# Performance work log

Hardware: AMD Instinct MI355X
Metric: run time of the kernel (lower is better)

Reference implementation:

```python
import jax, jax.numpy as jnp
import numpy as np
from math import ceil

N, C_IN, HV, WV = 4, 3, 256, 256
C, K, NUM_LAYERS = 16, 3, 10
HK, WK = 45, 45
PROX_SCALE, KSCALE, KBSCALE, EPS = 10.0, 100.0, 0.01, 1e-8


def conv2_same(x, w):
    # torch F.conv2d (cross-correlation) with 'same' padding
    return jax.lax.conv_general_dilated(x, w, (1, 1), 'SAME',
                                        dimension_numbers=('NCHW', 'OIHW', 'NCHW'))


def pad_to(x, size):
    h, w = x.shape[-2], x.shape[-1]
    pads = [(0, 0)] * (x.ndim - 2) + [(0, size[0] - h), (0, size[1] - w)]
    return jnp.pad(x, pads)


def soft_threshold(x, b):
    return jnp.sign(x) * jax.nn.relu(jnp.abs(x) - b)


def circ_shift(x, s):
    return jnp.roll(x, (-s[0], -s[1]), axis=(-2, -1))


def csq(c):
    return (c * jnp.conj(c)).real


def forward(blurred_image, w0, ws, biases, kernel_biases, kernel_proxes, zetas, eta):
    Nb, C_in, Hv, Wv = blurred_image.shape
    Hs, Ws = Hv + HK - 1, Wv + WK - 1
    Hb, Wb = Hs + HK - 1, Ws + WK - 1
    fft_size = (int(ceil(Hb / 64.0) * 64), int(ceil(Wb / 64.0) * 64))
    rfft = lambda x: jnp.fft.rfft2(x, s=fft_size, axes=(-2, -1))
    irfft = lambda X: jnp.fft.irfft2(X, s=fft_size, axes=(-2, -1))

    # first-layer filter: zero-mean per (out,in) filter, then spatial reflect
    w_mean = w0.reshape(C, C_in, -1).mean(axis=-1)
    w0c = w0 - w_mean[:, :, None, None]
    w0_unreflected = jnp.transpose(w0c, (1, 0, 2, 3))   # (C_in, C, K, K)
    w0r = w0c[:, :, ::-1, ::-1]

    # analysis: cascade of convs, each feature stack padded to fft_size
    wy_list = []
    fy = blurred_image
    for layer in range(NUM_LAYERS):
        w = w0r if layer == 0 else ws[layer - 1]
        fy = conv2_same(fy, w)
        fy_p = pad_to(jnp.pad(fy, ((0, 0), (0, 0), (HK - 1, HK - 1), (WK - 1, WK - 1))), fft_size)
        wy_list.append(fy_p)

    delta = jnp.zeros((Nb, HK, WK), dtype=blurred_image.dtype).at[:, HK // 2, WK // 2].set(1.0)
    b0 = biases[0][None, :, None, None]
    z = soft_threshold(circ_shift(wy_list[-1], (HK // 2, WK // 2)), b0)
    Fz = rfft(z)
    k = delta
    Fg = None
    for layer in range(NUM_LAYERS):
        fy_p = wy_list.pop()
        Ffy = rfft(fy_p)                       # (N, C, H, Wf) complex
        Fk = rfft(k)[:, None]                  # (N, 1, H, Wf)
        zeta = PROX_SCALE * zetas[layer][None, :, None, None]
        num = zeta * (jnp.conj(Fk) * Ffy) + Fz
        den = zeta * csq(Fk) + 1.0
        Fg = num / (den + EPS)
        b = biases[layer + 1][None, :, None, None]
        z = soft_threshold(irfft(Fg), b)
        Fz = rfft(z)
        zk = kernel_proxes[layer]
        num_k = zk * jnp.sum(jnp.conj(Fz) * Ffy, axis=1) + Fk[:, 0]
        den_k = zk * jnp.sum(csq(Fz), axis=1) + 1.0
        k = irfft(num_k / (den_k + EPS))
        k_flat = k.reshape(Nb, -1)
        k_max = jax.scipy.special.logsumexp(k_flat * KSCALE, axis=-1) / KSCALE
        bk = KBSCALE * kernel_biases[layer]
        k = jax.nn.relu(k[:, :HK, :WK] - bk * k_max[:, None, None])
        k_sum = jnp.sum(k, axis=(1, 2), keepdims=True)
        k = (k + EPS * delta) / (k_sum + EPS)

    # final closed-form image solve in frequency domain (3-channel Cramer's rule)
    Fy = rfft(jnp.pad(blurred_image, ((0, 0), (0, 0), (HK - 1, HK - 1), (WK - 1, WK - 1))))
    Fk = rfft(k)                                # (N, H, Wf)
    Fw0 = rfft(circ_shift(pad_to(w0_unreflected, fft_size), (K // 2, K // 2)))  # (C_in, C, H, Wf)
    b_final = biases[NUM_LAYERS + 1][None, :, None, None]
    Fg = rfft(soft_threshold(irfft(Fg), b_final))

    eta_s = PROX_SCALE * eta[None, :, None, None]      # (1, C, 1, 1)
    Fwr, Fwg, Fwb = Fw0[0:1], Fw0[1:2], Fw0[2:3]       # (1, C, H, Wf)
    Fyr, Fyg, Fyb = Fy[:, 0], Fy[:, 1], Fy[:, 2]
    Fk_sq = csq(Fk)
    Crr = Fk_sq + jnp.sum(eta_s * csq(Fwr), axis=1)
    Cgg = Fk_sq + jnp.sum(eta_s * csq(Fwg), axis=1)
    Cbb = Fk_sq + jnp.sum(eta_s * csq(Fwb), axis=1)
    Crg = jnp.sum(eta_s * jnp.conj(Fwr) * Fwg, axis=1)
    Crb = jnp.sum(eta_s * jnp.conj(Fwr) * Fwb, axis=1)
    Cgb = jnp.sum(eta_s * jnp.conj(Fwg) * Fwb, axis=1)
    Fk_conj = jnp.conj(Fk)
    Br = Fk_conj * Fyr + jnp.sum(eta_s * jnp.conj(Fwr) * Fg, axis=1)
    Bg = Fk_conj * Fyg + jnp.sum(eta_s * jnp.conj(Fwg) * Fg, axis=1)
    Bb = Fk_conj * Fyb + jnp.sum(eta_s * jnp.conj(Fwb) * Fg, axis=1)
    Crg_sq, Crb_sq, Cgb_sq = csq(Crg), csq(Crb), csq(Cgb)
    Irr = Cgg * Cbb - Cgb_sq
    Igg = Crr * Cbb - Crb_sq
    Ibb = Crr * Cgg - Crg_sq
    Irg = jnp.conj(Cgb) * Crb - Cbb * Crg
    Irb = Crg * Cgb - Cgg * Crb
    Igb = jnp.conj(Crg) * Crb - Crr * Cgb
    den = (Crr * (Cgg * Cbb - Cgb_sq) - Cgg * Crb_sq - Cbb * Crg_sq
           + 2 * (Crg * Cgb * jnp.conj(Crb)).real) + EPS
    Fxr = Irr * Br + Irg * Bg + Irb * Bb
    Fxg = jnp.conj(Irg) * Br + Igg * Bg + Igb * Bb
    Fxb = jnp.conj(Irb) * Br + jnp.conj(Igb) * Bg + Ibb * Bb
    Fx = jnp.stack([Fxr, Fxg, Fxb], axis=1) / den[:, None]

    image = irfft(Fx)[:, :, HK // 2:HK // 2 + Hv, WK // 2:WK // 2 + Wv]
    return image, k


def setup_inputs() -> dict:
    key = jax.random.key(0)
    ks = jax.random.split(key, 4)

    def xavier(k, shape, fan_in, fan_out):
        std = (2.0 / (fan_in + fan_out)) ** 0.5
        return std * jax.random.normal(k, shape, dtype=jnp.float32)

    return {
        'blurred_image': jax.random.normal(ks[0], (N, C_IN, HV, WV), dtype=jnp.float32),
        'w0': xavier(ks[1], (C, C_IN, K, K), C_IN * K * K, C * K * K),
        'ws': xavier(ks[2], (NUM_LAYERS - 1, C, C, 3, 3), C * 9, C * 9),
        'biases': jnp.full((NUM_LAYERS + 2, C), 0.02, dtype=jnp.float32),
        'kernel_biases': jnp.zeros((NUM_LAYERS,), dtype=jnp.float32),
        'kernel_proxes': jnp.ones((NUM_LAYERS,), dtype=jnp.float32),
        'zetas': jnp.ones((NUM_LAYERS, C), dtype=jnp.float32),
        'eta': jnp.ones((C,), dtype=jnp.float32),
    }


def reference(blurred_image, w0, ws, biases, kernel_biases, kernel_proxes, zetas, eta):
    return forward(blurred_image, w0, ws, biases, kernel_biases, kernel_proxes, zetas, eta)
```

## Files before the change

kernel.cpp:

```cpp
#include <hip/hip_runtime.h>
#include <math.h>

#define FH 384
#define KF 193
#define SPW 147456

typedef __attribute__((ext_vector_type(8))) short short8;
typedef __attribute__((ext_vector_type(4))) float f32x4;
typedef unsigned int u32;
typedef unsigned short u16;

static __device__ __forceinline__ float softt(float v, float b) {
    return copysignf(fmaxf(fabsf(v) - b, 0.f), v);
}
static __device__ __forceinline__ u16 bf16_rn(float v) {
    u32 u = __float_as_uint(v);
    u32 r = (u + 0x7FFFu + ((u >> 16) & 1u)) >> 16;
    return (u16)r;
}
static __device__ __forceinline__ float bf16_to_f(u16 h) {
    return __uint_as_float(((u32)h) << 16);
}
static __device__ __forceinline__ float2 ldc(const uint2* __restrict__ S, size_t i) {
    uint2 u = S[i];
    float2 r;
    r.x = __uint_as_float((u.x & 0xffffu) << 16) + __uint_as_float((u.y & 0xffffu) << 16);
    r.y = __uint_as_float(u.x & 0xffff0000u) + __uint_as_float(u.y & 0xffff0000u);
    return r;
}
static __device__ __forceinline__ float2 ldcu(uint2 u) {
    float2 r;
    r.x = __uint_as_float((u.x & 0xffffu) << 16) + __uint_as_float((u.y & 0xffffu) << 16);
    r.y = __uint_as_float(u.x & 0xffff0000u) + __uint_as_float(u.y & 0xffff0000u);
    return r;
}
static __device__ __forceinline__ uint2 packc(float re, float im) {
    u16 hr = bf16_rn(re), hi = bf16_rn(im);
    u16 lr = bf16_rn(re - bf16_to_f(hr)), li = bf16_rn(im - bf16_to_f(hi));
    uint2 o; o.x = (u32)hr | ((u32)hi << 16); o.y = (u32)lr | ((u32)li << 16);
    return o;
}
static __device__ __forceinline__ float2 cmul(float2 a, float2 b) {
    float2 r; r.x = a.x*b.x - a.y*b.y; r.y = a.x*b.y + a.y*b.x; return r;
}

__global__ void init_ef_k(float2* Ef) {
    int idx = blockIdx.x * 256 + threadIdx.x;
    if (idx >= FH * FH) return;
    int h = idx / FH, j = idx % FH;
    int m = (h * j) % FH;
    float th = (float)(6.283185307179586 / FH) * (float)m;
    float2 v; v.x = cosf(th); v.y = -sinf(th);
    Ef[idx] = v;
}

__global__ void init_tw(float2* twT) {
    int i = blockIdx.x * 256 + threadIdx.x;
    if (i < 193) {
        float th = (float)(6.283185307179586 / 384.0) * (float)i;
        float2 v; v.x = cosf(th); v.y = sinf(th);
        twT[i] = v;
    }
}

__global__ void init_e96(u16* __restrict__ H, u16* __restrict__ L, int inv)
{
    int idx = blockIdx.x * 256 + threadIdx.x;
    if (idx >= 192 * 192) return;
    int gm = idx / 192, kp = idx % 192;
    int m = gm >> 1, comp = gm & 1;
    int t = kp >> 1, ri = kp & 1;
    int mm = (m * t) % 96;
    float th = (float)(6.283185307179586 / 96.0) * (float)mm;
    float c = cosf(th), s = sinf(th);
    float er, ei;
    if (inv) { er = c * (1.f/384.f); ei = s * (1.f/384.f); }
    else     { er = c;               ei = -s; }
    float v;
    if (comp == 0) v = (ri == 0) ? er : -ei;
    else           v = (ri == 0) ? ei :  er;
    u16 h = bf16_rn(v);
    H[idx] = h;
    L[idx] = bf16_rn(v - bf16_to_f(h));
}

__global__ void init_t192(u16* __restrict__ H, u16* __restrict__ L)
{
    int idx = blockIdx.x * 256 + threadIdx.x;
    if (idx >= 208 * 192) return;
    int n = idx / 192, m = idx % 192;
    float v = 0.f;
    if (n < 194) {
        int j = n >> 1, ri = n & 1;
        int mm = (j * m) % 192;
        float th = (float)(6.283185307179586 / 192.0) * (float)mm;
        v = ri ? -sinf(th) : cosf(th);
    }
    u16 h = bf16_rn(v);
    H[idx] = h;
    L[idx] = bf16_rn(v - bf16_to_f(h));
}

__global__ void init_u192(u16* __restrict__ H, u16* __restrict__ L)
{
    int idx = blockIdx.x * 256 + threadIdx.x;
    if (idx >= 192 * 224) return;
    int m = idx / 224, kk = idx % 224;
    float v = 0.f;
    if (kk < 194) {
        int j = kk >> 1, ri = kk & 1;
        float cj = (j == 0 || j == 96) ? (1.f/384.f) : (2.f/384.f);
        int mm = (j * m) % 192;
        float th = (float)(6.283185307179586 / 192.0) * (float)mm;
        v = ri ? -cj*sinf(th) : cj*cosf(th);
    }
    u16 h = bf16_rn(v);
    H[idx] = h;
    L[idx] = bf16_rn(v - bf16_to_f(h));
}

__global__ void w0c_kernel(const float* __restrict__ w0, float* __restrict__ w0c) {
    int t = threadIdx.x;
    if (t < 48) {
        float m = 0.f;
        for (int d = 0; d < 9; ++d) m += w0[t*9+d];
        m *= (1.f/9.f);
        for (int d = 0; d < 9; ++d) w0c[t*9+d] = w0[t*9+d] - m;
    }
}

__global__ __launch_bounds__(256) void conv3x3_kernel(
    const float* __restrict__ inpF0, const u16* __restrict__ inH0, const u16* __restrict__ inL0,
    const float* __restrict__ w,
    u16* __restrict__ outH0, u16* __restrict__ outL0, int Cin, int flip,
    size_t inImgStride)
{
    size_t iofs = (size_t)blockIdx.z * inImgStride;
    const float* inF = inpF0 ? inpF0 + iofs : nullptr;
    const u16*   iH  = inH0 ? inH0 + iofs : nullptr;
    const u16*   iL  = inL0 ? inL0 + iofs : nullptr;
    u16* oH = outH0 + (size_t)blockIdx.z * 16*65536;
    u16* oL = outL0 + (size_t)blockIdx.z * 16*65536;
    __shared__ float tile[18][19];
    __shared__ float wl[16*16*9];
    int x0 = blockIdx.x * 16, y0 = blockIdx.y * 16;
    int t = threadIdx.x;
    int tx = t & 15, ty = t >> 4;
    int nw = 16 * Cin * 9;
    for (int i = t; i < nw; i += 256) {
        int d = i % 9;
        wl[i] = flip ? w[i + 8 - 2*d] : w[i];
    }
    float acc[16];
#pragma unroll
    for (int co = 0; co < 16; ++co) acc[co] = 0.f;
    for (int ci = 0; ci < Cin; ++ci) {
        __syncthreads();
        for (int i = t; i < 18*18; i += 256) {
            int yy = i / 18, xx = i % 18;
            int gy = y0 - 1 + yy, gx = x0 - 1 + xx;
            float v = 0.f;
            if (gy >= 0 && gy < 256 && gx >= 0 && gx < 256) {
                size_t ii;
                if (inF) ii = ((size_t)ci*256 + gy)*256 + gx;
                else     ii = ((size_t)ci*256 + gy)*256 + ((gx>>1) + (gx&1)*128);
                v = inF ? inF[ii] : (bf16_to_f(iH[ii]) + bf16_to_f(iL[ii]));
            }
            tile[yy][xx] = v;
        }
        __syncthreads();
        float v[9];
#pragma unroll
        for (int dy = 0; dy < 3; dy++)
#pragma unroll
            for (int dx = 0; dx < 3; dx++) v[dy*3+dx] = tile[ty+dy][tx+dx];
#pragma unroll
        for (int co = 0; co < 16; co++) {
            const float* wp = &wl[(co*Cin+ci)*9];
            acc[co] += v[0]*wp[0]+v[1]*wp[1]+v[2]*wp[2]
                     + v[3]*wp[3]+v[4]*wp[4]+v[5]*wp[5]
                     + v[6]*wp[6]+v[7]*wp[7]+v[8]*wp[8];
        }
    }
    int xo = x0 + tx;
    int xd = (xo >> 1) + (xo & 1)*128;
#pragma unroll
    for (int co = 0; co < 16; co++) {
        size_t o = ((size_t)co*256 + (y0+ty))*256 + xd;
        u16 h = bf16_rn(acc[co]);
        oH[o] = h;
        oL[o] = bf16_rn(acc[co] - bf16_to_f(h));
    }
}

__global__ void zinit_kernel(const u16* __restrict__ fy9H, const u16* __restrict__ fy9L,
                             const float* __restrict__ b0,
                             u16* __restrict__ oH, u16* __restrict__ oL, int total)
{
    int idx = blockIdx.x*256 + threadIdx.x;
    if (idx >= total) return;
    int x = idx % FH; int r = idx / FH; int y = r % FH; int plane = r / FH;
    int c = plane & 15;
    int Y = y + 22; if (Y >= FH) Y -= FH;
    int X = x + 22; if (X >= FH) X -= FH;
    int yy = Y - 44, xx = X - 44;
    float v = 0.f;
    if (yy >= 0 && yy < 256 && xx >= 0 && xx < 256) {
        size_t ii = ((size_t)plane*256 + yy)*256 + ((xx>>1) + (xx&1)*128);
        v = bf16_to_f(fy9H[ii]) + bf16_to_f(fy9L[ii]);
    }
    float s = softt(v, b0[c]);
    u16 h = bf16_rn(s);
    size_t d = (size_t)plane*SPW + (size_t)y*FH + ((x>>1) + (x&1)*192);
    oH[d] = h;
    oL[d] = bf16_rn(s - bf16_to_f(h));
}

static __device__ __forceinline__ void r2c192_epilogue(
    f32x4 accA[2][4], f32x4 accB[2][4],
    int col0, int njN, int y0, int wave, int lm, int lq,
    const float2* __restrict__ twT,
    uint2* __restrict__ outp, int B, int plane)
{
#pragma unroll
    for (int mi = 0; mi < 2; ++mi) {
#pragma unroll
// ... 230 lines not shown
    int idx = blockIdx.x*256 + threadIdx.x;
    if (idx >= rows * 97) return;
    int j = idx % 97;
    size_t b = (size_t)(idx / 97) * KF;
    if (j == 96) {
        float2 f = ldc(S, b + 96);
        S[b + 96] = packc(2.f*f.x, -2.f*f.y);
    } else {
        float2 f1 = ldc(S, b + j);
        float2 f2 = ldc(S, b + 192 - j);
        float gpx = f1.x + f2.x, gpy = f1.y - f2.y;
        float hx  = f1.x - f2.x, hy  = f1.y + f2.y;
        float2 tw = twT[j];
        float gmx = tw.x*hx - tw.y*hy;
        float gmy = tw.x*hy + tw.y*hx;
        S[b + j]       = packc(gpx, gpy);
        S[b + 192 - j] = packc(gmx, gmy);
    }
}

template<bool FUSE_LSE>
__global__ __launch_bounds__(256) void c2r192(
    const uint2* __restrict__ Ain,
    const u16* __restrict__ UH, const u16* __restrict__ UL,
    float* __restrict__ outp, const float* __restrict__ thr,
    u16* __restrict__ spH, u16* __restrict__ spL, int B,
    float2* __restrict__ parts)
{
    __shared__ u16 AhS[2][8*64*8];
    __shared__ u16 AlS[2][8*64*8];
    int col0 = blockIdx.x * 64;
    int y0   = blockIdx.y * 128;
    int plane = blockIdx.z;
    int tid = threadIdx.x;
    int wave = tid >> 6, lane = tid & 63;
    int lm = lane & 15, lq = lane >> 4;
    f32x4 accP[2][4], accQ[2][4];
#pragma unroll
    for (int mi = 0; mi < 2; ++mi)
#pragma unroll
        for (int nj = 0; nj < 4; ++nj) {
            accP[mi][nj] = (f32x4){0.f,0.f,0.f,0.f};
            accQ[mi][nj] = (f32x4){0.f,0.f,0.f,0.f};
        }
    for (int kt = 0; kt < 194; kt += 32) {
#pragma unroll
        for (int s = 0; s < 8; ++s) {
            int slot = tid + s*256;
            int p   = slot >> 10;
            int inr = slot & 1023;
            int r = inr >> 3, kq = inr & 7;
            size_t rowb = ((size_t)(y0 + r)*B + plane)*KF;
            int j0 = (kt + kq*4) >> 1;
            uint2 u0, u1;
            u0.x = u0.y = u1.x = u1.y = 0u;
            if (p == 0) {
                if (j0 < 96) u0 = Ain[rowb + j0];
                else if (j0 == 96) {
                    uint2 t = Ain[rowb + 96];
                    u0.x = t.x & 0xffffu; u0.y = t.y & 0xffffu;
                }
                if (j0 + 1 < 96) u1 = Ain[rowb + j0 + 1];
            } else {
                if (j0 < 96) u0 = Ain[rowb + 192 - j0];
                else if (j0 == 96) {
                    uint2 t = Ain[rowb + 96];
                    u0.x = t.x >> 16; u0.y = t.y >> 16;
                }
                if (j0 + 1 < 96) u1 = Ain[rowb + 191 - j0];
            }
            int base = ((r >> 4)*64 + (r & 15) + 16*(kq >> 1))*8 + (kq & 1)*4;
            uint2 hp, lp;
            hp.x = u0.x; hp.y = u1.x;
            lp.x = u0.y; lp.y = u1.y;
            *(uint2*)&AhS[p][base] = hp;
            *(uint2*)&AlS[p][base] = lp;
        }
        __syncthreads();
        short8 A0h[2], A0l[2], A1h[2], A1l[2];
#pragma unroll
        for (int mi = 0; mi < 2; ++mi) {
            int fo = ((wave*2 + mi)*64 + lane)*8;
            A0h[mi] = *(const short8*)&AhS[0][fo];
            A0l[mi] = *(const short8*)&AlS[0][fo];
            A1h[mi] = *(const short8*)&AhS[1][fo];
            A1l[mi] = *(const short8*)&AlS[1][fo];
        }
#pragma unroll
        for (int nj = 0; nj < 4; ++nj) {
            size_t toff = (size_t)(col0 + nj*16 + lm)*224 + kt + lq*8;
            short8 Bh = *(const short8*)(UH + toff);
            short8 Bl = *(const short8*)(UL + toff);
#pragma unroll
            for (int mi = 0; mi < 2; ++mi) {
                accP[mi][nj] = __builtin_amdgcn_mfma_f32_16x16x32_bf16(A0h[mi], Bh, accP[mi][nj], 0, 0, 0);
                accP[mi][nj] = __builtin_amdgcn_mfma_f32_16x16x32_bf16(A0h[mi], Bl, accP[mi][nj], 0, 0, 0);
                accP[mi][nj] = __builtin_amdgcn_mfma_f32_16x16x32_bf16(A0l[mi], Bh, accP[mi][nj], 0, 0, 0);
                accQ[mi][nj] = __builtin_amdgcn_mfma_f32_16x16x32_bf16(A1h[mi], Bh, accQ[mi][nj], 0, 0, 0);
                accQ[mi][nj] = __builtin_amdgcn_mfma_f32_16x16x32_bf16(A1h[mi], Bl, accQ[mi][nj], 0, 0, 0);
                accQ[mi][nj] = __builtin_amdgcn_mfma_f32_16x16x32_bf16(A1l[mi], Bh, accQ[mi][nj], 0, 0, 0);
            }
        }
        __syncthreads();
    }
    float bthr = thr ? thr[plane & 15] : 0.f;
    float lm_ = -1e30f, ls_ = 0.f;
#pragma unroll
    for (int mi = 0; mi < 2; ++mi) {
#pragma unroll
        for (int nj = 0; nj < 4; ++nj) {
            int m = col0 + nj*16 + lm;
#pragma unroll
            for (int rr = 0; rr < 4; ++rr) {
                int y = y0 + wave*32 + mi*16 + lq*4 + rr;
                float xe = accP[mi][nj][rr];
                float xo = accQ[mi][nj][rr];
                float2 o2; o2.x = xe; o2.y = xo;
                *(float2*)&outp[((size_t)plane*FH + y)*FH + 2*m] = o2;
                if (spH) {
                    float s0 = softt(xe, bthr), s1 = softt(xo, bthr);
                    u16 h0 = bf16_rn(s0), h1 = bf16_rn(s1);
                    u16 l0 = bf16_rn(s0 - bf16_to_f(h0)), l1 = bf16_rn(s1 - bf16_to_f(h1));
                    size_t d = (size_t)plane*SPW + (size_t)y*FH + m;
                    spH[d]       = h0; spL[d]       = l0;
                    spH[d + 192] = h1; spL[d + 192] = l1;
                }
                if (FUSE_LSE) {
                    lse_comb(lm_, ls_, 100.f*xe, 1.f);
                    lse_comb(lm_, ls_, 100.f*xo, 1.f);
                }
            }
        }
    }
    if (FUSE_LSE) {
        __shared__ float sm[256], ss[256];
        sm[tid] = lm_; ss[tid] = ls_;
        __syncthreads();
        for (int st = 128; st > 0; st >>= 1) {
            if (tid < st) {
                float mm = sm[tid], sc = ss[tid];
                lse_comb(mm, sc, sm[tid+st], ss[tid+st]);
                sm[tid] = mm; ss[tid] = sc;
            }
            __syncthreads();
        }
        if (tid == 0) {
            float2 o; o.x = sm[0]; o.y = ss[0];
            parts[plane*9 + blockIdx.y*3 + blockIdx.x] = o;
        }
    }
}

template<bool FUSE_FG>
__global__ __launch_bounds__(256) void zgemm_col_mfma4(
    const u16* __restrict__ EH, const u16* __restrict__ EL,
    const uint2* __restrict__ Bm, uint2* __restrict__ Cm, int N, float sgn,
    int ktHi, const float2* __restrict__ twT,
    uint2* __restrict__ FzFg, const uint2* __restrict__ FkB,
    const float* __restrict__ zet16, int GKF)
{
    __shared__ u16 BhS[4][4*64*8];
    __shared__ u16 BlS[4][4*64*8];
    int col0 = blockIdx.x * 64;
    int row0 = blockIdx.y * 64;
    int tid = threadIdx.x;
    int wave = tid >> 6, lane = tid & 63;
    int lm = lane & 15, lq = lane >> 4;
    f32x4 acc[4][4];
#pragma unroll
    for (int p = 0; p < 4; ++p)
#pragma unroll
        for (int nj = 0; nj < 4; ++nj)
            acc[p][nj] = (f32x4){0.f,0.f,0.f,0.f};
    int arow = row0 + wave*16 + lm;
    for (int kt = 0; kt < ktHi; kt += 32) {
        int tbase = kt >> 1;
#pragma unroll
        for (int s = 0; s < 8; ++s) {
            int slot = tid + s*256;
            int p    = slot >> 9;
            int inr  = slot & 511;
            int pair = inr >> 6;
            int n    = inr & 63;
            int gn   = col0 + n;
            int t0   = tbase + pair*2;
            uint2 u0, u1;
            u0.x = u0.y = u1.x = u1.y = 0u;
            if (gn < N) {
                u0 = Bm[(size_t)(4*t0 + p)*N + gn];
                u1 = Bm[(size_t)(4*t0 + 4 + p)*N + gn];
            }
            int ntile = n >> 4, n0 = n & 15;
            int lrow  = (pair >> 1)*16 + n0;
            int base  = (ntile*64 + lrow)*8 + (pair & 1)*4;
            uint2 hp, lp;
            hp.x = u0.x; hp.y = u1.x;
            lp.x = u0.y; lp.y = u1.y;
            *(uint2*)&BhS[p][base] = hp;
            *(uint2*)&BlS[p][base] = lp;
        }
        __syncthreads();
        short8 Ah, Al;
        {
            size_t aoff = (size_t)arow*192 + kt + lq*8;
            Ah = *(const short8*)(EH + aoff);
            Al = *(const short8*)(EL + aoff);
        }
#pragma unroll
        for (int nj = 0; nj < 4; ++nj) {
#pragma unroll
            for (int p = 0; p < 4; ++p) {
                short8 Bh = *(const short8*)&BhS[p][(nj*64 + lane)*8];
                short8 Bl = *(const short8*)&BlS[p][(nj*64 + lane)*8];
                acc[p][nj] = __builtin_amdgcn_mfma_f32_16x16x32_bf16(Ah, Bh, acc[p][nj], 0, 0, 0);
                acc[p][nj] = __builtin_amdgcn_mfma_f32_16x16x32_bf16(Ah, Bl, acc[p][nj], 0, 0, 0);
                acc[p][nj] = __builtin_amdgcn_mfma_f32_16x16x32_bf16(Al, Bh, acc[p][nj], 0, 0, 0);
            }
        }
        __syncthreads();
    }
#pragma unroll
    for (int nj = 0; nj < 4; ++nj) {
        int coln = col0 + nj*16 + lm;
        if (coln < N) {
            int r0 = row0 + wave*16 + lq*4;
            int h0b = r0 >> 1;
            int kk = 0, imgI = 0;
            float zeta = 0.f;
            if (FUSE_FG) {
                int planeI = coln / KF;
                kk = coln - planeI*KF;
                imgI = planeI >> 4;
                zeta = 10.f * zet16[planeI & 15];
            }
#pragma unroll
            for (int pp = 0; pp < 2; ++pp) {
                int h0 = h0b + pp;
                float2 c0, c1, c2, c3;
                c0.x = acc[0][nj][2*pp]; c0.y = acc[0][nj][2*pp+1];
                c1.x = acc[1][nj][2*pp]; c1.y = acc[1][nj][2*pp+1];
                c2.x = acc[2][nj][2*pp]; c2.y = acc[2][nj][2*pp+1];
                c3.x = acc[3][nj][2*pp]; c3.y = acc[3][nj][2*pp+1];
                float2 w1; { float2 t = twT[h0]; w1.x = t.x; w1.y = sgn*t.y; }
                float2 w2 = cmul(w1, w1);
                float2 w3 = cmul(w2, w1);
                float2 d1 = cmul(c1, w1);
                float2 d2 = cmul(c2, w2);
                float2 d3 = cmul(c3, w3);
                float2 s02, m02, s13, m13, i13;
                s02.x = c0.x + d2.x; s02.y = c0.y + d2.y;
                m02.x = c0.x - d2.x; m02.y = c0.y - d2.y;
                s13.x = d1.x + d3.x; s13.y = d1.y + d3.y;
                m13.x = d1.x - d3.x; m13.y = d1.y - d3.y;
                i13.x = -sgn*m13.y;  i13.y = sgn*m13.x;
                float2 X[4];
                X[0].x = s02.x + s13.x; X[0].y = s02.y + s13.y;
                X[2].x = s02.x - s13.x; X[2].y = s02.y - s13.y;
                X[1].x = m02.x + i13.x; X[1].y = m02.y + i13.y;
                X[3].x = m02.x - i13.x; X[3].y = m02.y - i13.y;
#pragma unroll
                for (int q = 0; q < 4; ++q) {
                    int row = h0 + 96*q;
                    uint2 px = packc(X[q].x, X[q].y);
                    Cm[(size_t)row*N + coln] = px;
                    if (FUSE_FG) {
                        float2 fy = ldcu(px);
                        float2 fz = ldc(FzFg, (size_t)row*N + coln);
                        float2 fk = ldc(FkB, (size_t)row*GKF + imgI*KF + kk);
                        float nx = zeta*(fk.x*fy.x + fk.y*fy.y) + fz.x;
                        float ny = zeta*(fk.x*fy.y - fk.y*fy.x) + fz.y;
                        float den = zeta*(fk.x*fk.x + fk.y*fk.y) + 1.f + 1e-8f;
                        float inv = 1.f/den;
                        FzFg[(size_t)row*N + coln] = packc(nx*inv, ny*inv);
                    }
                }
            }
        }
    }
}

__global__ void knum_kernel(const uint2* __restrict__ Fz, const uint2* __restrict__ Ffy,
                            const uint2* __restrict__ Fk, const float* __restrict__ kprox,
                            int L, int total, uint2* __restrict__ outk)
{
    int idx = blockIdx.x*256 + threadIdx.x;
    if (idx >= total) return;
    int k = idx % KF; int r = idx / KF;
    float zk = kprox[L];
    float s1x = 0.f, s1y = 0.f, s2 = 0.f;
    for (int c = 0; c < 16; ++c) {
        size_t bi = ((size_t)r*16 + c)*KF + k;
        float2 fz = ldc(Fz, bi), fy = ldc(Ffy, bi);
        s1x += fz.x*fy.x + fz.y*fy.y;
        s1y += fz.x*fy.y - fz.y*fy.x;
        s2  += fz.x*fz.x + fz.y*fz.y;
    }
    float2 fk = ldc(Fk, idx);
    float nx = zk*s1x + fk.x, ny = zk*s1y + fk.y;
    float den = zk*s2 + 1.f + 1e-8f;
    float inv = 1.f/den;
    outk[idx] = packc(nx*inv, ny*inv);
}

__global__ void zero_kernel(float* __restrict__ p, int n)
{
    int i = blockIdx.x*256 + threadIdx.x;
    if (i < n) p[i] = 0.f;
}

__global__ void kdelta_kernel(float* __restrict__ kful, int G)
{
    int t = threadIdx.x;
    if (t < G) kful[(size_t)t*FH*FH + 22*FH + 22] = 1.f;
}

__global__ __launch_bounds__(256) void knew_kernel(const float2* __restrict__ parts,
    const float* __restrict__ kraw0, const float* __restrict__ kb, int L,
    float* __restrict__ kful0)
{
    int img = blockIdx.x;
    const float* kraw = kraw0 + (size_t)img*FH*FH;
    float*       kful = kful0 + (size_t)img*FH*FH;
    int t = threadIdx.x;
    __shared__ float sm[16], ss[16];
    if (t < 16) {
        if (t < 9) { float2 p = parts[img*9 + t]; sm[t] = p.x; ss[t] = p.y; }
        else       { sm[t] = -1e30f; ss[t] = 0.f; }
    }
    __syncthreads();
    for (int st = 8; st > 0; st >>= 1) {
        if (t < st) {
            float mm = sm[t], sc = ss[t];
            lse_comb(mm, sc, sm[t+st], ss[t+st]);
            sm[t] = mm; ss[t] = sc;
        }
        __syncthreads();
    }
    float kmax = (sm[0] + logf(ss[0])) * 0.01f;
    float thr = 0.01f * kb[L] * kmax;
    float vs[8]; float loc = 0.f;
#pragma unroll
    for (int ii = 0; ii < 8; ++ii) {
        int i = t + ii*256;
        float v = 0.f;
        if (i < 45*45) {
            int y = i/45, x = i - y*45;
            v = fmaxf(kraw[y*FH + x] - thr, 0.f);
        }
        vs[ii] = v; loc += v;
    }
    __shared__ float sr[256];
    sr[t] = loc; __syncthreads();
    for (int st = 128; st > 0; st >>= 1) { if (t < st) sr[t] += sr[t+st]; __syncthreads(); }
    float den = sr[0] + 1e-8f;
#pragma unroll
    for (int ii = 0; ii < 8; ++ii) {
        int i = t + ii*256;
        if (i < 45*45) {
            int y = i/45, x = i - y*45;
            float v = vs[ii] + ((y == 22 && x == 22) ? 1e-8f : 0.f);
            kful[y*FH + x] = v / den;
        }
    }
}

__global__ void fw0_kernel(const float* __restrict__ w0c, const float2* __restrict__ Ef,
                           float2* __restrict__ Fw0)
{
    int idx = blockIdx.x*256 + threadIdx.x;
    if (idx >= 48*FH*KF) return;
    int k = idx % KF; int r = idx / KF;
    int c = r & 15; int r2 = r >> 4;
    int ci = r2 % 3; int h = r2 / 3;
    float accx = 0.f, accy = 0.f;
#pragma unroll
    for (int ky = 0; ky < 3; ++ky) {
        int a1 = ky - 1; if (a1 < 0) a1 += FH;
        float2 e1 = Ef[h*FH + a1];
#pragma unroll
        for (int kx = 0; kx < 3; ++kx) {
            int a2 = kx - 1; if (a2 < 0) a2 += FH;
            float2 e2 = Ef[k*FH + a2];
            float wv = w0c[((c*3 + ci)*3 + ky)*3 + kx];
            float tr = e1.x*e2.x - e1.y*e2.y;
            float ti = e1.x*e2.y + e1.y*e2.x;
            accx += wv*tr; accy += wv*ti;
        }
    }
    float2 o; o.x = accx; o.y = accy;
    Fw0[idx] = o;
}

__global__ void wiener_kernel(const uint2* __restrict__ Fk, const uint2* __restrict__ Fy,
    const float2* __restrict__ Fw0, const uint2* __restrict__ Fg2,
    const float* __restrict__ eta, int G, int total, uint2* __restrict__ Fx)
{
    int idx = blockIdx.x*256 + threadIdx.x;
    if (idx >= total) return;
    int k = idx % KF; int r = idx / KF;
    int h = r / G;
    float2 fk = ldc(Fk, idx);
    float fksq = fk.x*fk.x + fk.y*fk.y;
    float2 fyr = ldc(Fy, ((size_t)3*r + 0)*KF + k);
    float2 fyg = ldc(Fy, ((size_t)3*r + 1)*KF + k);
    float2 fyb = ldc(Fy, ((size_t)3*r + 2)*KF + k);
    float Crr = fksq, Cgg = fksq, Cbb = fksq;
    float2 Crg, Crb, Cgb;
    Crg.x = Crg.y = Crb.x = Crb.y = Cgb.x = Cgb.y = 0.f;
    float2 Br, Bg, Bb;
    Br.x = fk.x*fyr.x + fk.y*fyr.y; Br.y = fk.x*fyr.y - fk.y*fyr.x;
    Bg.x = fk.x*fyg.x + fk.y*fyg.y; Bg.y = fk.x*fyg.y - fk.y*fyg.x;
    Bb.x = fk.x*fyb.x + fk.y*fyb.y; Bb.y = fk.x*fyb.y - fk.y*fyb.x;
    for (int c = 0; c < 16; ++c) {
        float es = 10.f * eta[c];
        float2 wr = Fw0[((size_t)h*48 +  0 + c)*KF + k];
        float2 wg = Fw0[((size_t)h*48 + 16 + c)*KF + k];
        float2 wb = Fw0[((size_t)h*48 + 32 + c)*KF + k];
        float2 g  = ldc(Fg2, ((size_t)r*16 + c)*KF + k);
        Crr += es*(wr.x*wr.x + wr.y*wr.y);
        Cgg += es*(wg.x*wg.x + wg.y*wg.y);
        Cbb += es*(wb.x*wb.x + wb.y*wb.y);
        Crg.x += es*(wr.x*wg.x + wr.y*wg.y); Crg.y += es*(wr.x*wg.y - wr.y*wg.x);
        Crb.x += es*(wr.x*wb.x + wr.y*wb.y); Crb.y += es*(wr.x*wb.y - wr.y*wb.x);
        Cgb.x += es*(wg.x*wb.x + wg.y*wb.y); Cgb.y += es*(wg.x*wb.y - wg.y*wb.x);
        Br.x += es*(wr.x*g.x + wr.y*g.y); Br.y += es*(wr.x*g.y - wr.y*g.x);
        Bg.x += es*(wg.x*g.x + wg.y*g.y); Bg.y += es*(wg.x*g.y - wg.y*g.x);
        Bb.x += es*(wb.x*g.x + wb.y*g.y); Bb.y += es*(wb.x*g.y - wb.y*g.x);
    }
    float Crg_sq = Crg.x*Crg.x + Crg.y*Crg.y;
    float Crb_sq = Crb.x*Crb.x + Crb.y*Crb.y;
    float Cgb_sq = Cgb.x*Cgb.x + Cgb.y*Cgb.y;
    float Irr = Cgg*Cbb - Cgb_sq;
    float Igg = Crr*Cbb - Crb_sq;
    float Ibb = Crr*Cgg - Crg_sq;
    float2 Irg, Irb, Igb;
    Irg.x = (Cgb.x*Crb.x + Cgb.y*Crb.y) - Cbb*Crg.x;
    Irg.y = (Cgb.x*Crb.y - Cgb.y*Crb.x) - Cbb*Crg.y;
    Irb.x = (Crg.x*Cgb.x - Crg.y*Cgb.y) - Cgg*Crb.x;
    Irb.y = (Crg.x*Cgb.y + Crg.y*Cgb.x) - Cgg*Crb.y;
    Igb.x = (Crg.x*Crb.x + Crg.y*Crb.y) - Crr*Cgb.x;
    Igb.y = (Crg.x*Crb.y - Crg.y*Crb.x) - Crr*Cgb.y;
    float tx_ = Crg.x*Cgb.x - Crg.y*Cgb.y;
    float ty_ = Crg.x*Cgb.y + Crg.y*Cgb.x;
    float den = Crr*Irr - Cgg*Crb_sq - Cbb*Crg_sq + 2.f*(tx_*Crb.x + ty_*Crb.y) + 1e-8f;
    float inv = 1.f/den;
    float ox, oy;
    ox = (Irr*Br.x + (Irg.x*Bg.x - Irg.y*Bg.y) + (Irb.x*Bb.x - Irb.y*Bb.y))*inv;
    oy = (Irr*Br.y + (Irg.x*Bg.y + Irg.y*Bg.x) + (Irb.x*Bb.y + Irb.y*Bb.x))*inv;
    Fx[((size_t)3*r + 0)*KF + k] = packc(ox, oy);
    ox = ((Irg.x*Br.x + Irg.y*Br.y) + Igg*Bg.x + (Igb.x*Bb.x - Igb.y*Bb.y))*inv;
    oy = ((Irg.x*Br.y - Irg.y*Br.x) + Igg*Bg.y + (Igb.x*Bb.y + Igb.y*Bb.x))*inv;
    Fx[((size_t)3*r + 1)*KF + k] = packc(ox, oy);
    ox = ((Irb.x*Br.x + Irb.y*Br.y) + (Igb.x*Bg.x + Igb.y*Bg.y) + Ibb*Bb.x)*inv;
    oy = ((Irb.x*Br.y - Irb.y*Br.x) + (Igb.x*Bg.y - Igb.y*Bg.x) + Ibb*Bb.y)*inv;
    Fx[((size_t)3*r + 2)*KF + k] = packc(ox, oy);
}

__global__ void crop_kernel(const float* __restrict__ sp, float* __restrict__ outp, int total)
{
    int idx = blockIdx.x*256 + threadIdx.x;
    if (idx >= total) return;
    int x = idx & 255; int r = idx >> 8; int y = r & 255; int plane = r >> 8;
    outp[idx] = sp[((size_t)plane*FH + (y+22))*FH + (x+22)];
}

__global__ void kcopy_kernel(const float* __restrict__ kful, float* __restrict__ outp, int total)
{
    int idx = blockIdx.x*256 + threadIdx.x;
    if (idx >= total) return;
    int rem = idx % 2025; int img = idx / 2025;
    int x = rem % 45; int y = rem / 45;
    outp[idx] = kful[(size_t)img*FH*FH + y*FH + x];
}

extern "C" void kernel_launch(void* const* d_in, const int* in_sizes, int n_in,
                              void* d_out, int out_size, void* d_ws, size_t ws_size,
                              hipStream_t stream)
{
    (void)in_sizes; (void)n_in; (void)out_size;
    const float* blurred = (const float*)d_in[0];
    const float* w0      = (const float*)d_in[1];
    const float* wsw     = (const float*)d_in[2];
    const float* biases  = (const float*)d_in[3];
    const float* kbias   = (const float*)d_in[4];
    const float* kprox   = (const float*)d_in[5];
    const float* zetas   = (const float*)d_in[6];
    const float* eta     = (const float*)d_in[7];
    float* outp = (float*)d_out;

    auto al = [](size_t b) { return (b + 255) & ~(size_t)255; };
    auto need = [&](int G) -> size_t {
        size_t s = 0;
        s += al((size_t)FH*FH*8);
        s += al(193*8);
        s += 4*al((size_t)192*192*2);
        s += 2*al((size_t)208*192*2);
        s += 2*al((size_t)192*224*2);
        s += al(432*4);
        s += 2*al((size_t)10*G*16*65536*2);
        s += al((size_t)G*16*FH*FH*4);
        s += 2*al((size_t)G*16*SPW*2);
        s += 3*al((size_t)G*16*FH*KF*8);
        s += 4*al((size_t)G*FH*KF*8);
        s += 2*al((size_t)G*FH*FH*4);
        s += 2*al((size_t)G*3*FH*KF*8);
        s += al((size_t)G*64*8);
        return s;
    };
    int G = 4;
    while (G > 1 && need(G) > ws_size) G >>= 1;

    char* base = (char*)d_ws;
    size_t off = 0;
    auto alloc = [&](size_t bytes) -> void* {
        void* p = (void*)(base + off);
        off += (bytes + 255) & ~(size_t)255;
        return p;
    };
    float2* Ef   = (float2*)alloc((size_t)FH*FH*8);
    float2* twT  = (float2*)alloc(193*8);
    u16* EfH = (u16*)alloc((size_t)192*192*2);
    u16* EfL = (u16*)alloc((size_t)192*192*2);
    u16* EiH = (u16*)alloc((size_t)192*192*2);
    u16* EiL = (u16*)alloc((size_t)192*192*2);
    u16* T1H = (u16*)alloc((size_t)208*192*2);
    u16* T1L = (u16*)alloc((size_t)208*192*2);
    u16* U1H = (u16*)alloc((size_t)192*224*2);
    u16* U1L = (u16*)alloc((size_t)192*224*2);
    float*  w0cB = (float*)alloc(432*4);
    u16*    fyH  = (u16*)alloc((size_t)10*G*16*65536*2);
    u16*    fyL  = (u16*)alloc((size_t)10*G*16*65536*2);
    float*  zsp  = (float*)alloc((size_t)G*16*FH*FH*4);
    u16*    zspSH= (u16*)alloc((size_t)G*16*SPW*2);
    u16*    zspSL= (u16*)alloc((size_t)G*16*SPW*2);
    uint2*  mid  = (uint2*)alloc((size_t)G*16*FH*KF*8);
    uint2*  FzFg = (uint2*)alloc((size_t)G*16*FH*KF*8);
    uint2*  Ffy  = (uint2*)alloc((size_t)G*16*FH*KF*8);
    uint2*  Fk   = (uint2*)alloc((size_t)G*FH*KF*8);
    uint2*  kfA  = (uint2*)alloc((size_t)G*FH*KF*8);
    uint2*  kfB  = (uint2*)alloc((size_t)G*FH*KF*8);
    uint2*  kmid = (uint2*)alloc((size_t)G*FH*KF*8);
    float*  kraw = (float*)alloc((size_t)G*FH*FH*4);
    float*  kful = (float*)alloc((size_t)G*FH*FH*4);
    uint2*  FyB  = (uint2*)alloc((size_t)G*3*FH*KF*8);
    uint2*  FxB  = (uint2*)alloc((size_t)G*3*FH*KF*8);
    float2* lseP = (float2*)alloc((size_t)G*64*8);
    float2* Fw0B = (float2*)fyH;

    init_ef_k<<<(FH*FH+255)/256, 256, 0, stream>>>(Ef);
    init_tw<<<1, 256, 0, stream>>>(twT);
    init_e96<<<(192*192+255)/256, 256, 0, stream>>>(EfH, EfL, 0);
    init_e96<<<(192*192+255)/256, 256, 0, stream>>>(EiH, EiL, 1);
    init_t192<<<(208*192+255)/256, 256, 0, stream>>>(T1H, T1L);
    init_u192<<<(192*224+255)/256, 256, 0, stream>>>(U1H, U1L);
    w0c_kernel<<<1, 64, 0, stream>>>(w0, w0cB);

    auto zgf = [&](const uint2* Bm, uint2* Cm, int Ncols) {
        zgemm_col_mfma4<false><<<dim3((Ncols+63)/64, 3), 256, 0, stream>>>(
            EfH, EfL, Bm, Cm, Ncols, -1.f, 192, twT, nullptr, nullptr, nullptr, 0);
    };
    auto zgi = [&](const uint2* Bm, uint2* Cm, int Ncols) {
        zgemm_col_mfma4<false><<<dim3((Ncols+63)/64, 3), 256, 0, stream>>>(
            EiH, EiL, Bm, Cm, Ncols, 1.f, 192, twT, nullptr, nullptr, nullptr, 0);
    };
    auto r2c = [&](const float* inp, int inH, int inW, int oY, int oX,
                   const float* thr, uint2* o, int B) {
        r2c192_f<<<dim3(4, 3, B), 256, 0, stream>>>(
            inp, inH, inW, inW, (size_t)inH*inW, oY, oX, thr, T1H, T1L, twT, o, B);
    };
    auto r2cs = [&](const u16* Hs, const u16* Ls, int inH, int inW, int oY, int oX,
                    uint2* o, int B) {
        r2c192_s<<<dim3(4, 3, B), 256, 0, stream>>>(
            Hs, Ls, inH, inW, oY, oX, T1H, T1L, twT, o, B);
    };
    auto c2r = [&](uint2* Ain, float* o, int B,
                   const float* thr, u16* sH, u16* sL) {
        int rows = FH * B;
        gpm_kernel<<<(rows*97 + 255)/256, 256, 0, stream>>>(Ain, twT, rows);
        c2r192<false><<<dim3(3, 3, B), 256, 0, stream>>>(
            Ain, U1H, U1L, o, thr, sH, sL, B, nullptr);
    };
    auto c2rk = [&](uint2* Ain, float* o, int B, float2* parts) {
        int rows = FH * B;
        gpm_kernel<<<(rows*97 + 255)/256, 256, 0, stream>>>(Ain, twT, rows);
        c2r192<true><<<dim3(3, 3, B), 256, 0, stream>>>(
            Ain, U1H, U1L, o, nullptr, nullptr, nullptr, B, parts);
    };
    auto r2ck = [&]() {
        r2c192_f<<<dim3(4, 1, G), 256, 0, stream>>>(
            kful, 45, 45, FH, (size_t)FH*FH, 0, 0, nullptr, T1H, T1L, twT, kmid, G);
        zgemm_col_mfma4<false><<<dim3((G*KF+63)/64, 3), 256, 0, stream>>>(
            EfH, EfL, kmid, Fk, G*KF, -1.f, 32, twT, nullptr, nullptr, nullptr, 0);
    };

    const size_t CKL = (size_t)G*16*65536;

    for (int g0 = 0; g0 < 4; g0 += G) {
        const float* img = blurred + (size_t)g0*3*65536;

        conv3x3_kernel<<<dim3(16,16,G), 256, 0, stream>>>(
            img, nullptr, nullptr, w0cB, fyH, fyL, 3, 1, (size_t)3*65536);
        for (int l = 1; l < 10; ++l)
            conv3x3_kernel<<<dim3(16,16,G), 256, 0, stream>>>(
                nullptr, fyH + (size_t)(l-1)*CKL, fyL + (size_t)(l-1)*CKL,
                wsw + (size_t)(l-1)*2304,
                fyH + (size_t)l*CKL, fyL + (size_t)l*CKL, 16, 0, (size_t)16*65536);

        int totZ = G*16*FH*FH;
        zinit_kernel<<<(totZ+255)/256, 256, 0, stream>>>(
            fyH + 9*CKL, fyL + 9*CKL, biases, zspSH, zspSL, totZ);
        r2cs(zspSH, zspSL, FH, FH, 0, 0, mid, G*16);
        zgf(mid, FzFg, G*16*KF);

        zero_kernel<<<(G*FH*FH+255)/256, 256, 0, stream>>>(kful, G*FH*FH);
        kdelta_kernel<<<1, 64, 0, stream>>>(kful, G);

        int totK = G*FH*KF;
        int NS = G*16*KF;
        for (int it = 0; it < 10; ++it) {
            int Lfy = 9 - it;
            r2ck();
            r2cs(fyH + (size_t)Lfy*CKL, fyL + (size_t)Lfy*CKL, 256, 256, 44, 44, mid, G*16);
            zgemm_col_mfma4<true><<<dim3((NS+63)/64, 3), 256, 0, stream>>>(
                EfH, EfL, mid, Ffy, NS, -1.f, 192, twT,
                FzFg, Fk, zetas + it*16, G*KF);
            zgi(FzFg, mid, NS);
            c2r(mid, zsp, G*16, biases + (it+1)*16, zspSH, zspSL);
            r2cs(zspSH, zspSL, FH, FH, 0, 0, mid, G*16);
            zgf(mid, FzFg, NS);
            knum_kernel<<<(totK+255)/256, 256, 0, stream>>>(FzFg, Ffy, Fk, kprox, it, totK, kfA);
            zgi(kfA, kfB, G*KF);
            c2rk(kfB, kraw, G, lseP);
            knew_kernel<<<G, 256, 0, stream>>>(lseP, kraw, kbias, it, kful);
        }

        r2c(img, 256, 256, 44, 44, nullptr, mid, 3*G);
        zgf(mid, FyB, 3*G*KF);
        r2ck();
        r2c(zsp, FH, FH, 0, 0, biases + 11*16, mid, G*16);
        zgf(mid, FzFg, G*16*KF);
        fw0_kernel<<<(48*FH*KF+255)/256, 256, 0, stream>>>(w0cB, Ef, Fw0B);
        wiener_kernel<<<(totK+255)/256, 256, 0, stream>>>(Fk, FyB, Fw0B, FzFg, eta, G, totK, FxB);
        zgi(FxB, mid, 3*G*KF);
        c2r(mid, zsp, 3*G, nullptr, nullptr, nullptr);
        int totC = G*3*65536;
        crop_kernel<<<(totC+255)/256, 256, 0, stream>>>(zsp, outp + (size_t)g0*3*65536, totC);
        int totKC = G*2025;
        kcopy_kernel<<<(totKC+255)/256, 256, 0, stream>>>(kful, outp + 786432 + g0*2025, totKC);
    }
}
```

Baseline: 8.136 ms.

## Switch column FFT from 96x4 to 48x8 mixed-radix decomposition

The column-direction 384-point DFT is restructured from a 96-point dense DFT done as an MFMA GEMM plus a radix-4 twiddle stage to a 48-point dense GEMM plus a radix-8 butterfly stage. This halves the K-dimension of the bf16 split-precision GEMM, cutting MFMA work and DFT-matrix traffic, at the cost of a larger butterfly epilogue with more twiddle loads. Tile shapes move to 48x32 blocks with 192 threads, and the twiddle table grows to all 384 entries. The ktHi=32 path for the kernel FFT is kept and still covers the nonzero kernel rows.

```diff
diff --git a/kernel.cpp b/kernel.cpp
--- a/kernel.cpp
+++ b/kernel.cpp
@@ -56,22 +56,22 @@
 
 __global__ void init_tw(float2* twT) {
     int i = blockIdx.x * 256 + threadIdx.x;
-    if (i < 193) {
+    if (i < 384) {
         float th = (float)(6.283185307179586 / 384.0) * (float)i;
         float2 v; v.x = cosf(th); v.y = sinf(th);
         twT[i] = v;
     }
 }
 
-__global__ void init_e96(u16* __restrict__ H, u16* __restrict__ L, int inv)
+__global__ void init_e48(u16* __restrict__ H, u16* __restrict__ L, int inv)
 {
     int idx = blockIdx.x * 256 + threadIdx.x;
-    if (idx >= 192 * 192) return;
-    int gm = idx / 192, kp = idx % 192;
+    if (idx >= 96 * 96) return;
+    int gm = idx / 96, kp = idx % 96;
     int m = gm >> 1, comp = gm & 1;
     int t = kp >> 1, ri = kp & 1;
-    int mm = (m * t) % 96;
-    float th = (float)(6.283185307179586 / 96.0) * (float)mm;
+    int mm = (m * t) % 48;
+    float th = (float)(6.283185307179586 / 48.0) * (float)mm;
     float c = cosf(th), s = sinf(th);
     float er, ei;
     if (inv) { er = c * (1.f/384.f); ei = s * (1.f/384.f); }
@@ -608,43 +608,41 @@
 }
 
 template<bool FUSE_FG>
-__global__ __launch_bounds__(256) void zgemm_col_mfma4(
+__global__ __launch_bounds__(192) void zgemm_col_mfma8(
     const u16* __restrict__ EH, const u16* __restrict__ EL,
     const uint2* __restrict__ Bm, uint2* __restrict__ Cm, int N, float sgn,
     int ktHi, const float2* __restrict__ twT,
     uint2* __restrict__ FzFg, const uint2* __restrict__ FkB,
     const float* __restrict__ zet16, int GKF)
 {
-    __shared__ u16 BhS[4][4*64*8];
-    __shared__ u16 BlS[4][4*64*8];
-    int col0 = blockIdx.x * 64;
-    int row0 = blockIdx.y * 64;
+    __shared__ u16 BhS[8][2*64*8];
+    __shared__ u16 BlS[8][2*64*8];
+    int col0 = blockIdx.x * 32;
+    int row0 = blockIdx.y * 48;
     int tid = threadIdx.x;
     int wave = tid >> 6, lane = tid & 63;
     int lm = lane & 15, lq = lane >> 4;
-    f32x4 acc[4][4];
-#pragma unroll
-    for (int p = 0; p < 4; ++p)
-#pragma unroll
-        for (int nj = 0; nj < 4; ++nj)
+    f32x4 acc[8][2];
+#pragma unroll
+    for (int p = 0; p < 8; ++p)
+#pragma unroll
+        for (int nj = 0; nj < 2; ++nj)
             acc[p][nj] = (f32x4){0.f,0.f,0.f,0.f};
     int arow = row0 + wave*16 + lm;
     for (int kt = 0; kt < ktHi; kt += 32) {
         int tbase = kt >> 1;
-#pragma unroll
-        for (int s = 0; s < 8; ++s) {
-            int slot = tid + s*256;
-            int p    = slot >> 9;
-            int inr  = slot & 511;
-            int pair = inr >> 6;
-            int n    = inr & 63;
+        for (int slot = tid; slot < 2048; slot += 192) {
+            int p    = slot >> 8;
+            int inr  = slot & 255;
+            int pair = inr >> 5;
+            int n    = inr & 31;
             int gn   = col0 + n;
             int t0   = tbase + pair*2;
             uint2 u0, u1;
             u0.x = u0.y = u1.x = u1.y = 0u;
             if (gn < N) {
-                u0 = Bm[(size_t)(4*t0 + p)*N + gn];
-                u1 = Bm[(size_t)(4*t0 + 4 + p)*N + gn];
+                u0 = Bm[(size_t)(8*t0 + p)*N + gn];
+                u1 = Bm[(size_t)(8*t0 + 8 + p)*N + gn];
             }
             int ntile = n >> 4, n0 = n & 15;
             int lrow  = (pair >> 1)*16 + n0;
@@ -658,14 +656,14 @@
         __syncthreads();
         short8 Ah, Al;
         {
-            size_t aoff = (size_t)arow*192 + kt + lq*8;
+            size_t aoff = (size_t)arow*96 + kt + lq*8;
             Ah = *(const short8*)(EH + aoff);
             Al = *(const short8*)(EL + aoff);
         }
 #pragma unroll
-        for (int nj = 0; nj < 4; ++nj) {
-#pragma unroll
-            for (int p = 0; p < 4; ++p) {
+        for (int nj = 0; nj < 2; ++nj) {
+#pragma unroll
+            for (int p = 0; p < 8; ++p) {
                 short8 Bh = *(const short8*)&BhS[p][(nj*64 + lane)*8];
                 short8 Bl = *(const short8*)&BlS[p][(nj*64 + lane)*8];
                 acc[p][nj] = __builtin_amdgcn_mfma_f32_16x16x32_bf16(Ah, Bh, acc[p][nj], 0, 0, 0);
@@ -675,8 +673,9 @@
         }
         __syncthreads();
     }
-#pragma unroll
-    for (int nj = 0; nj < 4; ++nj) {
+    const float rt = 0.70710678118654752f;
+#pragma unroll
+    for (int nj = 0; nj < 2; ++nj) {
         int coln = col0 + nj*16 + lm;
         if (coln < N) {
             int r0 = row0 + wave*16 + lq*4;
@@ -692,31 +691,52 @@
 #pragma unroll
             for (int pp = 0; pp < 2; ++pp) {
                 int h0 = h0b + pp;
-                float2 c0, c1, c2, c3;
-                c0.x = acc[0][nj][2*pp]; c0.y = acc[0][nj][2*pp+1];
-                c1.x = acc[1][nj][2*pp]; c1.y = acc[1][nj][2*pp+1];
-                c2.x = acc[2][nj][2*pp]; c2.y = acc[2][nj][2*pp+1];
-                c3.x = acc[3][nj][2*pp]; c3.y = acc[3][nj][2*pp+1];
-                float2 w1; { float2 t = twT[h0]; w1.x = t.x; w1.y = sgn*t.y; }
-                float2 w2 = cmul(w1, w1);
-                float2 w3 = cmul(w2, w1);
-                float2 d1 = cmul(c1, w1);
-                float2 d2 = cmul(c2, w2);
-                float2 d3 = cmul(c3, w3);
+                float2 d[8];
+                d[0].x = acc[0][nj][2*pp]; d[0].y = acc[0][nj][2*pp+1];
+#pragma unroll
+                for (int p = 1; p < 8; ++p) {
+                    float2 w = twT[p*h0];
+                    w.y *= sgn;
+                    float2 c; c.x = acc[p][nj][2*pp]; c.y = acc[p][nj][2*pp+1];
+                    d[p] = cmul(c, w);
+                }
+                float2 e0, e1, e2, e3, o0, o1, o2, o3;
+                e0.x = d[0].x + d[4].x; e0.y = d[0].y + d[4].y;
+                e1.x = d[1].x + d[5].x; e1.y = d[1].y + d[5].y;
+                e2.x = d[2].x + d[6].x; e2.y = d[2].y + d[6].y;
+                e3.x = d[3].x + d[7].x; e3.y = d[3].y + d[7].y;
+                o0.x = d[0].x - d[4].x; o0.y = d[0].y - d[4].y;
+                o1.x = d[1].x - d[5].x; o1.y = d[1].y - d[5].y;
+                o2.x = d[2].x - d[6].x; o2.y = d[2].y - d[6].y;
+                o3.x = d[3].x - d[7].x; o3.y = d[3].y - d[7].y;
                 float2 s02, m02, s13, m13, i13;
-                s02.x = c0.x + d2.x; s02.y = c0.y + d2.y;
-                m02.x = c0.x - d2.x; m02.y = c0.y - d2.y;
-                s13.x = d1.x + d3.x; s13.y = d1.y + d3.y;
-                m13.x = d1.x - d3.x; m13.y = d1.y - d3.y;
+                s02.x = e0.x + e2.x; s02.y = e0.y + e2.y;
+                m02.x = e0.x - e2.x; m02.y = e0.y - e2.y;
+                s13.x = e1.x + e3.x; s13.y = e1.y + e3.y;
+                m13.x = e1.x - e3.x; m13.y = e1.y - e3.y;
                 i13.x = -sgn*m13.y;  i13.y = sgn*m13.x;
-                float2 X[4];
+                float2 X[8];
                 X[0].x = s02.x + s13.x; X[0].y = s02.y + s13.y;
-                X[2].x = s02.x - s13.x; X[2].y = s02.y - s13.y;
-                X[1].x = m02.x + i13.x; X[1].y = m02.y + i13.y;
-                X[3].x = m02.x - i13.x; X[3].y = m02.y - i13.y;
-#pragma unroll
-                for (int q = 0; q < 4; ++q) {
-                    int row = h0 + 96*q;
+                X[4].x = s02.x - s13.x; X[4].y = s02.y - s13.y;
+                X[2].x = m02.x + i13.x; X[2].y = m02.y + i13.y;
+                X[6].x = m02.x - i13.x; X[6].y = m02.y - i13.y;
+                float2 g0 = o0, g1, g2, g3;
+                g1.x = rt*(o1.x - sgn*o1.y);  g1.y = rt*(sgn*o1.x + o1.y);
+                g2.x = -sgn*o2.y;             g2.y = sgn*o2.x;
+                g3.x = rt*(-(o3.x + sgn*o3.y)); g3.y = rt*(sgn*o3.x - o3.y);
+                float2 sp, mp, sq, mq, iq;
+                sp.x = g0.x + g2.x; sp.y = g0.y + g2.y;
+                mp.x = g0.x - g2.x; mp.y = g0.y - g2.y;
+                sq.x = g1.x + g3.x; sq.y = g1.y + g3.y;
+                mq.x = g1.x - g3.x; mq.y = g1.y - g3.y;
+                iq.x = -sgn*mq.y;   iq.y = sgn*mq.x;
+                X[1].x = sp.x + sq.x; X[1].y = sp.y + sq.y;
+                X[5].x = sp.x - sq.x; X[5].y = sp.y - sq.y;
+                X[3].x = mp.x + iq.x; X[3].y = mp.y + iq.y;
+                X[7].x = mp.x - iq.x; X[7].y = mp.y - iq.y;
+#pragma unroll
+                for (int q = 0; q < 8; ++q) {
+                    int row = h0 + 48*q;
                     uint2 px = packc(X[q].x, X[q].y);
                     Cm[(size_t)row*N + coln] = px;
                     if (FUSE_FG) {
@@ -948,8 +968,8 @@
     auto need = [&](int G) -> size_t {
         size_t s = 0;
         s += al((size_t)FH*FH*8);
-        s += al(193*8);
-        s += 4*al((size_t)192*192*2);
+        s += al(384*8);
+        s += 4*al((size_t)96*96*2);
         s += 2*al((size_t)208*192*2);
         s += 2*al((size_t)192*224*2);
         s += al(432*4);
@@ -974,11 +994,11 @@
         return p;
     };
     float2* Ef   = (float2*)alloc((size_t)FH*FH*8);
-    float2* twT  = (float2*)alloc(193*8);
-    u16* EfH = (u16*)alloc((size_t)192*192*2);
-    u16* EfL = (u16*)alloc((size_t)192*192*2);
-    u16* EiH = (u16*)alloc((size_t)192*192*2);
-    u16* EiL = (u16*)alloc((size_t)192*192*2);
+    float2* twT  = (float2*)alloc(384*8);
+    u16* EfH = (u16*)alloc((size_t)96*96*2);
+    u16* EfL = (u16*)alloc((size_t)96*96*2);
+    u16* EiH = (u16*)alloc((size_t)96*96*2);
+    u16* EiL = (u16*)alloc((size_t)96*96*2);
     u16* T1H = (u16*)alloc((size_t)208*192*2);
     u16* T1L = (u16*)alloc((size_t)208*192*2);
     u16* U1H = (u16*)alloc((size_t)192*224*2);
@@ -1004,20 +1024,20 @@
     float2* Fw0B = (float2*)fyH;
 
     init_ef_k<<<(FH*FH+255)/256, 256, 0, stream>>>(Ef);
-    init_tw<<<1, 256, 0, stream>>>(twT);
-    init_e96<<<(192*192+255)/256, 256, 0, stream>>>(EfH, EfL, 0);
-    init_e96<<<(192*192+255)/256, 256, 0, stream>>>(EiH, EiL, 1);
+    init_tw<<<2, 256, 0, stream>>>(twT);
+    init_e48<<<(96*96+255)/256, 256, 0, stream>>>(EfH, EfL, 0);
+    init_e48<<<(96*96+255)/256, 256, 0, stream>>>(EiH, EiL, 1);
     init_t192<<<(208*192+255)/256, 256, 0, stream>>>(T1H, T1L);
     init_u192<<<(192*224+255)/256, 256, 0, stream>>>(U1H, U1L);
     w0c_kernel<<<1, 64, 0, stream>>>(w0, w0cB);
 
     auto zgf = [&](const uint2* Bm, uint2* Cm, int Ncols) {
-        zgemm_col_mfma4<false><<<dim3((Ncols+63)/64, 3), 256, 0, stream>>>(
-            EfH, EfL, Bm, Cm, Ncols, -1.f, 192, twT, nullptr, nullptr, nullptr, 0);
+        zgemm_col_mfma8<false><<<dim3((Ncols+31)/32, 2), 192, 0, stream>>>(
+            EfH, EfL, Bm, Cm, Ncols, -1.f, 96, twT, nullptr, nullptr, nullptr, 0);
     };
     auto zgi = [&](const uint2* Bm, uint2* Cm, int Ncols) {
-        zgemm_col_mfma4<false><<<dim3((Ncols+63)/64, 3), 256, 0, stream>>>(
-            EiH, EiL, Bm, Cm, Ncols, 1.f, 192, twT, nullptr, nullptr, nullptr, 0);
+        zgemm_col_mfma8<false><<<dim3((Ncols+31)/32, 2), 192, 0, stream>>>(
+            EiH, EiL, Bm, Cm, Ncols, 1.f, 96, twT, nullptr, nullptr, nullptr, 0);
     };
     auto r2c = [&](const float* inp, int inH, int inW, int oY, int oX,
                    const float* thr, uint2* o, int B) {
@@ -1045,7 +1065,7 @@
     auto r2ck = [&]() {
         r2c192_f<<<dim3(4, 1, G), 256, 0, stream>>>(
             kful, 45, 45, FH, (size_t)FH*FH, 0, 0, nullptr, T1H, T1L, twT, kmid, G);
-        zgemm_col_mfma4<false><<<dim3((G*KF+63)/64, 3), 256, 0, stream>>>(
+        zgemm_col_mfma8<false><<<dim3((G*KF+31)/32, 2), 192, 0, stream>>>(
             EfH, EfL, kmid, Fk, G*KF, -1.f, 32, twT, nullptr, nullptr, nullptr, 0);
     };
 
@@ -1077,8 +1097,8 @@
             int Lfy = 9 - it;
             r2ck();
             r2cs(fyH + (size_t)Lfy*CKL, fyL + (size_t)Lfy*CKL, 256, 256, 44, 44, mid, G*16);
-            zgemm_col_mfma4<true><<<dim3((NS+63)/64, 3), 256, 0, stream>>>(
-                EfH, EfL, mid, Ffy, NS, -1.f, 192, twT,
+            zgemm_col_mfma8<true><<<dim3((NS+31)/32, 2), 192, 0, stream>>>(
+                EfH, EfL, mid, Ffy, NS, -1.f, 96, twT,
                 FzFg, Fk, zetas + it*16, G*KF);
             zgi(FzFg, mid, NS);
             c2r(mid, zsp, G*16, biases + (it+1)*16, zspSH, zspSL);
```

After: 10.73 ms. +31.9%, slower.
